# Optimization experiments

Hardware: AMD Instinct MI355X
Metric: run time of the kernel (lower is better)

The kernel has to match this reference:

```python
import jax, jax.numpy as jnp
import numpy as np

B, C_IN, N = 16, 64, 8192
C_OUT, NUM_RING = 128, 8
EPS = 1e-5  # BatchNorm1d default


def setup_inputs() -> dict:
    key = jax.random.key(0)
    k1, k2, k3, k4 = jax.random.split(key, 4)
    x = jax.random.normal(k1, (B, C_IN, N), dtype=jnp.float32)
    ring = jax.random.randint(k2, (B, N), 0, NUM_RING, dtype=jnp.int32)
    W = jax.random.normal(k3, (NUM_RING, C_OUT, C_IN), dtype=jnp.float32) * 0.05
    b = jax.random.normal(k4, (NUM_RING, C_OUT), dtype=jnp.float32) * 0.05
    gamma = jnp.ones((NUM_RING, C_OUT), dtype=jnp.float32)
    beta = jnp.zeros((NUM_RING, C_OUT), dtype=jnp.float32)
    return {"x": x, "ring": ring, "W": W, "b": b, "gamma": gamma, "beta": beta}


def reference(x, ring, W, b, gamma, beta):
    Bb, C, Nn = x.shape
    num_ring = W.shape[0]
    M = Bb * Nn
    xf = x.transpose(0, 2, 1).reshape(M, C)      # [M, 64] point features
    rf = ring.reshape(M)                          # [M] ring id per point

    # Per-ring Conv1d(64->128, k=1): linear with ring-selected weights.
    # num_ring is small; masked dense GEMMs avoid gathering [M,128,64] weights.
    y = jnp.zeros((M, W.shape[1]), dtype=xf.dtype)
    for r in range(num_ring):
        yr = xf @ W[r].T + b[r]
        y = jnp.where((rf == r)[:, None], yr, y)  # [M, 128]

    # Training-mode BatchNorm1d per ring group: stats over all points of that
    # ring across all batches (BN sees [1,128,M_r]). Biased variance.
    cnt = jax.ops.segment_sum(jnp.ones((M,), y.dtype), rf, num_segments=num_ring)
    cnt = jnp.maximum(cnt, 1.0)[:, None]          # [R,1]
    s = jax.ops.segment_sum(y, rf, num_segments=num_ring)       # [R,128]
    ss = jax.ops.segment_sum(y * y, rf, num_segments=num_ring)  # [R,128]
    mean = s / cnt
    var = ss / cnt - mean * mean
    yn = (y - mean[rf]) * jax.lax.rsqrt(var[rf] + EPS) * gamma[rf] + beta[rf]

    # Segment max over (batch, ring) pairs, broadcast back to every point.
    bidx = jnp.repeat(jnp.arange(Bb, dtype=rf.dtype), Nn)        # [M]
    seg = bidx * num_ring + rf
    mx = jax.ops.segment_max(yn, seg, num_segments=Bb * num_ring)  # [B*R,128]
    out = mx[seg].reshape(Bb, Nn, -1).transpose(0, 2, 1)         # [B,128,N]
    return out
```

## Files before the change

kernel.cpp:

```cpp
#include <hip/hip_runtime.h>
#include <stdint.h>
#include <math.h>

#define B_    16
#define CIN   64
#define NPT   8192
#define COUT  128
#define NRING 8
#define EPSV  1e-5f
#define CAP   2048u
#define MBLK  6

typedef unsigned int uint32;
typedef unsigned short ushort;
typedef unsigned long long ull;
typedef short short8 __attribute__((ext_vector_type(8)));
typedef float floatx4 __attribute__((ext_vector_type(4)));

__device__ __forceinline__ uint32 fkey(float f) {
  uint32 u = __float_as_uint(f);
  return (u & 0x80000000u) ? ~u : (u | 0x80000000u);
}
__device__ __forceinline__ float kinv(uint32 k) {
  uint32 u = (k & 0x80000000u) ? (k ^ 0x80000000u) : ~k;
  return __uint_as_float(u);
}
__device__ __forceinline__ uint32 f2bf(float f) {
  uint32 u = __float_as_uint(f);
  return (u + 0x7fffu + ((u >> 16) & 1u)) >> 16;
}

__global__ __launch_bounds__(256) void k_init(
    const float* __restrict__ W, ushort* __restrict__ Wb,
    uint32* __restrict__ cursor,
    float* __restrict__ sums, float* __restrict__ ssums,
    uint32* __restrict__ mxkey, uint32* __restrict__ mnkey)
{
  int tid = threadIdx.x;
  int blk = blockIdx.x;
  if (blk < 32) {
    int idx0 = blk * 256 + tid;
    for (int idx = idx0; idx < B_ * NRING * COUT; idx += 32 * 256) {
      mxkey[idx] = 0u;
      mnkey[idx] = 0xFFFFFFFFu;
      if (idx < NRING * COUT) { sums[idx] = 0.f; ssums[idx] = 0.f; }
      if (idx < B_ * NRING)   cursor[idx] = (uint32)idx * CAP;
    }
  } else {
    int idx0 = (blk - 32) * 256 + tid;
    for (int idx = idx0; idx < NRING * COUT * CIN; idx += 8 * 256)
      Wb[idx] = (ushort)f2bf(W[idx]);
  }
}

__global__ __launch_bounds__(128) void k_scatter(
    const float* __restrict__ x, const int* __restrict__ ring,
    uint32* __restrict__ cursor, ushort* __restrict__ xsb)
{
  __shared__ uint32 xl2[64 * 33];
  __shared__ int    dstrow[64];
  __shared__ ushort rankl[64];
  __shared__ uint32 rcnt[NRING], rbase[NRING], rstart[NRING];

  int tid  = threadIdx.x;
  int lane = tid & 63;
  int w    = tid >> 6;
  int blk  = blockIdx.x;
  int b    = blk >> 7;
  int n0   = (blk & 127) * 64;

  if (w == 0) {
    int rl = ring[b * NPT + n0 + lane];
    uint32 wrank = 0;
    #pragma unroll
    for (int rr = 0; rr < NRING; ++rr) {
      ull m = __ballot(rl == rr);
      if (rl == rr) wrank = (uint32)__popcll(m & ((1ull << lane) - 1ull));
      if (lane == rr) rcnt[rr] = (uint32)__popcll(m);
    }
    if (lane < NRING) {
      rbase[lane] = atomicAdd(&cursor[b * NRING + lane], rcnt[lane]);
      uint32 s = 0;
      for (int rp = 0; rp < lane; ++rp) s += rcnt[rp];
      rstart[lane] = s;
    }
    int myrow = (int)(rstart[rl] + wrank);
    rankl[lane] = (ushort)myrow;
    uint32 gpos = rbase[rl] + wrank;
    uint32 limit = (uint32)(b * NRING + rl + 1) * CAP;
    dstrow[myrow] = (gpos < limit) ? (int)gpos : -1;
  }
  __syncthreads();

  const float* xb = x + (size_t)b * CIN * NPT + n0;
  uint32 myrank = rankl[lane];
  #pragma unroll
  for (int kp = 0; kp < 16; ++kp) {
    int k = w * 32 + kp * 2;
    float fa = xb[(size_t)k * NPT + lane];
    float fb = xb[(size_t)(k + 1) * NPT + lane];
    xl2[myrank * 33 + (k >> 1)] = f2bf(fa) | (f2bf(fb) << 16);
  }
  __syncthreads();

  uint2* dst = reinterpret_cast<uint2*>(xsb);
  #pragma unroll
  for (int i = 0; i < 8; ++i) {
    int w2 = tid + i * 128;
    int row = w2 >> 4;
    int p   = w2 & 15;
    int dr  = dstrow[row];
    if (dr >= 0) {
      uint2 v;
      v.x = xl2[row * 33 + 2 * p];
      v.y = xl2[row * 33 + 2 * p + 1];
      dst[(size_t)dr * 16 + p] = v;
    }
  }
}

__global__ __launch_bounds__(256) void k_main(
    const ushort* __restrict__ xsb, const ushort* __restrict__ Wb,
    const uint32* __restrict__ cursor,
    float* __restrict__ sums, float* __restrict__ ssums,
    uint32* __restrict__ mxkey, uint32* __restrict__ mnkey)
{
  int blk = blockIdx.x;
  int c4 = blk % MBLK;
  int r  = (blk / MBLK) & 7;
  int b  = blk / (MBLK * NRING);
  uint32 segBase = (uint32)(b * NRING + r) * CAP;
  uint32 segCnt  = __builtin_amdgcn_readfirstlane(
                       min(cursor[b * NRING + r] - segBase, CAP));

  int tid = threadIdx.x;
  int lane = tid & 63;
  int w = tid >> 6;
  uint32 m0 = (uint32)(c4 * 4 + w) * 64;
  if (m0 >= segCnt) return;

  int lm = lane & 15;
  int lk = lane >> 4;

  const ushort* wr = Wb + (size_t)r * COUT * CIN;
  short8 bfr[8][2];
  #pragma unroll
  for (int nt = 0; nt < 8; ++nt) {
    const ushort* wc = wr + (size_t)(nt * 16 + lm) * CIN + lk * 8;
    bfr[nt][0] = *reinterpret_cast<const short8*>(wc);
    bfr[nt][1] = *reinterpret_cast<const short8*>(wc + 32);
  }

  float s_[8], ss_[8], mx_[8], mn_[8];
  #pragma unroll
  for (int nt = 0; nt < 8; ++nt) {
    s_[nt] = 0.f; ss_[nt] = 0.f;
    mx_[nt] = -__builtin_inff(); mn_[nt] = __builtin_inff();
  }

  #pragma unroll
  for (int mt = 0; mt < 4; ++mt) {
    uint32 row_rel = m0 + (uint32)mt * 16 + (uint32)lm;
    bool valid = row_rel < segCnt;
    uint32 row_g = segBase + (valid ? row_rel : (segCnt - 1));
    const ushort* xr = xsb + (size_t)row_g * CIN + lk * 8;
    short8 a0 = *reinterpret_cast<const short8*>(xr);
    short8 a1 = *reinterpret_cast<const short8*>(xr + 32);
    if (!valid) { a0 = (short8)0; a1 = (short8)0; }

    #pragma unroll
    for (int nt = 0; nt < 8; ++nt) {
      floatx4 f = {0.f, 0.f, 0.f, 0.f};
      f = __builtin_amdgcn_mfma_f32_16x16x32_bf16(a0, bfr[nt][0], f, 0, 0, 0);
      f = __builtin_amdgcn_mfma_f32_16x16x32_bf16(a1, bfr[nt][1], f, 0, 0, 0);
      #pragma unroll
      for (int j = 0; j < 4; ++j) {
        bool vj = (m0 + (uint32)mt * 16 + (uint32)(lk * 4 + j)) < segCnt;
        float zv = f[j];
        s_[nt] += zv;
        ss_[nt] = fmaf(zv, zv, ss_[nt]);
        mx_[nt] = fmaxf(mx_[nt], vj ? zv : -__builtin_inff());
        mn_[nt] = fminf(mn_[nt], vj ? zv :  __builtin_inff());
      }
    }
  }

  #pragma unroll
  for (int nt = 0; nt < 8; ++nt) {
    float sv = s_[nt], qv = ss_[nt], Mv = mx_[nt], mv = mn_[nt];
    sv += __shfl_xor(sv, 16, 64); sv += __shfl_xor(sv, 32, 64);
    qv += __shfl_xor(qv, 16, 64); qv += __shfl_xor(qv, 32, 64);
    Mv = fmaxf(Mv, __shfl_xor(Mv, 16, 64)); Mv = fmaxf(Mv, __shfl_xor(Mv, 32, 64));
    mv = fminf(mv, __shfl_xor(mv, 16, 64)); mv = fminf(mv, __shfl_xor(mv, 32, 64));
    if (lane < 16) {
      int ch = nt * 16 + lane;
      atomicAdd(&sums [r * COUT + ch], sv);
      atomicAdd(&ssums[r * COUT + ch], qv);
      atomicMax(&mxkey[(b * NRING + r) * COUT + ch], fkey(Mv));
      atomicMin(&mnkey[(b * NRING + r) * COUT + ch], fkey(mv));
    }
  }
}

__global__ __launch_bounds__(256) void k_bcast(
    const int* __restrict__ ring, const uint32* __restrict__ cursor,
    const float* __restrict__ sums, const float* __restrict__ ssums,
    const uint32* __restrict__ mxkey, const uint32* __restrict__ mnkey,
    const float* __restrict__ gamma, const float* __restrict__ beta,
    float* __restrict__ out)
{
  __shared__ float mxl[NRING * 129];
  __shared__ float ringcnt[NRING];
  int tid = threadIdx.x;
  int blk = blockIdx.x;
  int b   = blk >> 7;
  int n0  = (blk & 127) * 64;

  if (tid < NRING) {
    uint32 t = 0;
    for (int bb = 0; bb < B_; ++bb)
      t += min(cursor[bb * NRING + tid] - (uint32)(bb * NRING + tid) * CAP, CAP);
    ringcnt[tid] = fmaxf((float)t, 1.f);
  }
  __syncthreads();

  for (int j = tid; j < NRING * COUT; j += 256) {
    int r = j >> 7, c = j & 127;
    float cnt  = ringcnt[r];
    float mean = sums[j] / cnt;
    float var  = fmaxf(ssums[j] / cnt - mean * mean, 0.f);
    float inv  = 1.f / sqrtf(var + EPSV);
    float a    = gamma[j] * inv;
    float bet  = beta[j];
    float zmax = kinv(mxkey[b * NRING * COUT + j]);
    float zmin = kinv(mnkey[b * NRING * COUT + j]);
    mxl[r * 129 + c] = (a >= 0.f) ? fmaf(a, zmax - mean, bet)
                                  : fmaf(a, zmin - mean, bet);
  }
  __syncthreads();

  int wv = tid >> 6, lane = tid & 63;
  int rl = ring[b * NPT + n0 + lane];
  float* ob = out + (size_t)b * COUT * NPT + n0 + lane;
  int roff = rl * 129;
  #pragma unroll 8
  for (int c = wv * 32; c < wv * 32 + 32; ++c) {
    ob[(size_t)c * NPT] = mxl[roff + c];
  }
}

extern "C" void kernel_launch(void* const* d_in, const int* in_sizes, int n_in,
                              void* d_out, int out_size, void* d_ws, size_t ws_size,
                              hipStream_t stream)
{
  const float* x     = (const float*)d_in[0];
  const int*   ring  = (const int*)  d_in[1];
  const float* W     = (const float*)d_in[2];
  const float* gamma = (const float*)d_in[4];
  const float* beta  = (const float*)d_in[5];
  float* out = (float*)d_out;

  ushort* Wb      = (ushort*)d_ws;
  uint32* cursor  = (uint32*)(Wb + 65536);
  float*  sums    = (float*)(cursor + 128);
  float*  ssums   = sums + 1024;
  uint32* mxkey   = (uint32*)(ssums + 1024);
  uint32* mnkey   = mxkey + 16384;

  ushort* xsb = (ushort*)out;

  k_init   <<<dim3(40),   dim3(256), 0, stream>>>(W, Wb, cursor, sums, ssums, mxkey, mnkey);
  k_scatter<<<dim3(2048), dim3(128), 0, stream>>>(x, ring, cursor, xsb);
  k_main   <<<dim3(B_ * NRING * MBLK), dim3(256), 0, stream>>>(xsb, Wb, cursor, sums, ssums, mxkey, mnkey);
  k_bcast  <<<dim3(2048), dim3(256), 0, stream>>>(ring, cursor, sums, ssums, mxkey, mnkey, gamma, beta, out);
}
```

Baseline: 63.35 us.

## Widen scatter and broadcast tiles to 256 points with vectorized float4 accesses

The scatter kernel now handles 256 points per block with 256 threads. Ring ranks are combined across four wavefronts through shared per-wave counts and offsets, so there are fewer cursor atomics per point. Global loads of x, stores of the bf16 rows, and the broadcast kernel's output writes now use 16-byte vector accesses. The broadcast kernel recomputes its BN/max table per block, and with 4x fewer blocks that redundant work shrinks. In exchange, shared-memory scatter writes may hit more bank conflicts, and the larger per-block LDS footprint lowers occupancy.

```diff
diff --git a/kernel.cpp b/kernel.cpp
--- a/kernel.cpp
+++ b/kernel.cpp
@@ -53,68 +53,89 @@
   }
 }
 
-__global__ __launch_bounds__(128) void k_scatter(
+__global__ __launch_bounds__(256) void k_scatter(
     const float* __restrict__ x, const int* __restrict__ ring,
     uint32* __restrict__ cursor, ushort* __restrict__ xsb)
 {
-  __shared__ uint32 xl2[64 * 33];
-  __shared__ int    dstrow[64];
-  __shared__ ushort rankl[64];
-  __shared__ uint32 rcnt[NRING], rbase[NRING], rstart[NRING];
+  __shared__ uint32 xl2[256 * 33];
+  __shared__ int    dstrow[256];
+  __shared__ ushort rankl[256];
+  __shared__ uint32 wcnt[4][NRING], woff[4][NRING];
+  __shared__ uint32 rbase[NRING], rstart[NRING];
 
   int tid  = threadIdx.x;
   int lane = tid & 63;
   int w    = tid >> 6;
   int blk  = blockIdx.x;
-  int b    = blk >> 7;
-  int n0   = (blk & 127) * 64;
-
-  if (w == 0) {
-    int rl = ring[b * NPT + n0 + lane];
-    uint32 wrank = 0;
-    #pragma unroll
+  int b    = blk >> 5;
+  int n0   = (blk & 31) * 256;
+
+  int rl = ring[b * NPT + n0 + tid];
+  uint32 wrank = 0, mycnt = 0;
+  #pragma unroll
+  for (int rr = 0; rr < NRING; ++rr) {
+    ull m = __ballot(rl == rr);
+    if (rl == rr) wrank = (uint32)__popcll(m & ((1ull << lane) - 1ull));
+    if (lane == rr) mycnt = (uint32)__popcll(m);
+  }
+  if (lane < NRING) wcnt[w][lane] = mycnt;
+  __syncthreads();
+  if (tid < NRING) {
+    uint32 t = wcnt[0][tid] + wcnt[1][tid] + wcnt[2][tid] + wcnt[3][tid];
+    rbase[tid] = atomicAdd(&cursor[b * NRING + tid], t);
+  }
+  if (tid == 0) {
+    uint32 acc = 0;
     for (int rr = 0; rr < NRING; ++rr) {
-      ull m = __ballot(rl == rr);
-      if (rl == rr) wrank = (uint32)__popcll(m & ((1ull << lane) - 1ull));
-      if (lane == rr) rcnt[rr] = (uint32)__popcll(m);
-    }
-    if (lane < NRING) {
-      rbase[lane] = atomicAdd(&cursor[b * NRING + lane], rcnt[lane]);
-      uint32 s = 0;
-      for (int rp = 0; rp < lane; ++rp) s += rcnt[rp];
-      rstart[lane] = s;
-    }
-    int myrow = (int)(rstart[rl] + wrank);
-    rankl[lane] = (ushort)myrow;
-    uint32 gpos = rbase[rl] + wrank;
+      rstart[rr] = acc;
+      uint32 o = acc;
+      #pragma unroll
+      for (int ww = 0; ww < 4; ++ww) { woff[ww][rr] = o; o += wcnt[ww][rr]; }
+      acc = o;
+    }
+  }
+  __syncthreads();
+  int myrow = (int)(woff[w][rl] + wrank);
+  rankl[tid] = (ushort)myrow;
+  {
+    uint32 gpos = rbase[rl] + ((uint32)myrow - rstart[rl]);
     uint32 limit = (uint32)(b * NRING + rl + 1) * CAP;
     dstrow[myrow] = (gpos < limit) ? (int)gpos : -1;
   }
   __syncthreads();
 
+  int myr0 = rankl[lane * 4 + 0];
+  int myr1 = rankl[lane * 4 + 1];
+  int myr2 = rankl[lane * 4 + 2];
+  int myr3 = rankl[lane * 4 + 3];
   const float* xb = x + (size_t)b * CIN * NPT + n0;
-  uint32 myrank = rankl[lane];
-  #pragma unroll
-  for (int kp = 0; kp < 16; ++kp) {
-    int k = w * 32 + kp * 2;
-    float fa = xb[(size_t)k * NPT + lane];
-    float fb = xb[(size_t)(k + 1) * NPT + lane];
-    xl2[myrank * 33 + (k >> 1)] = f2bf(fa) | (f2bf(fb) << 16);
-  }
-  __syncthreads();
-
-  uint2* dst = reinterpret_cast<uint2*>(xsb);
-  #pragma unroll
-  for (int i = 0; i < 8; ++i) {
-    int w2 = tid + i * 128;
-    int row = w2 >> 4;
-    int p   = w2 & 15;
+  #pragma unroll
+  for (int kp = 0; kp < 8; ++kp) {
+    int k0 = w * 16 + kp * 2;
+    float4 va = *reinterpret_cast<const float4*>(xb + (size_t)k0 * NPT + lane * 4);
+    float4 vb = *reinterpret_cast<const float4*>(xb + (size_t)(k0 + 1) * NPT + lane * 4);
+    int idx = k0 >> 1;
+    xl2[myr0 * 33 + idx] = f2bf(va.x) | (f2bf(vb.x) << 16);
+    xl2[myr1 * 33 + idx] = f2bf(va.y) | (f2bf(vb.y) << 16);
+    xl2[myr2 * 33 + idx] = f2bf(va.z) | (f2bf(vb.z) << 16);
+    xl2[myr3 * 33 + idx] = f2bf(va.w) | (f2bf(vb.w) << 16);
+  }
+  __syncthreads();
+
+  uint4* dst = reinterpret_cast<uint4*>(xsb);
+  #pragma unroll
+  for (int it = 0; it < 8; ++it) {
+    int slot = tid + it * 256;
+    int row = slot >> 3;
+    int p   = slot & 7;
     int dr  = dstrow[row];
     if (dr >= 0) {
-      uint2 v;
-      v.x = xl2[row * 33 + 2 * p];
-      v.y = xl2[row * 33 + 2 * p + 1];
-      dst[(size_t)dr * 16 + p] = v;
+      uint4 v;
+      v.x = xl2[row * 33 + 4 * p + 0];
+      v.y = xl2[row * 33 + 4 * p + 1];
+      v.z = xl2[row * 33 + 4 * p + 2];
+      v.w = xl2[row * 33 + 4 * p + 3];
+      dst[(size_t)dr * 8 + p] = v;
     }
   }
 }
@@ -213,8 +234,8 @@
   __shared__ float ringcnt[NRING];
   int tid = threadIdx.x;
   int blk = blockIdx.x;
-  int b   = blk >> 7;
-  int n0  = (blk & 127) * 64;
+  int b   = blk >> 5;
+  int n0  = (blk & 31) * 256;
 
   if (tid < NRING) {
     uint32 t = 0;
@@ -225,7 +246,7 @@
   __syncthreads();
 
   for (int j = tid; j < NRING * COUT; j += 256) {
-    int r = j >> 7, c = j & 127;
+    int r = j >> 7;
     float cnt  = ringcnt[r];
     float mean = sums[j] / cnt;
     float var  = fmaxf(ssums[j] / cnt - mean * mean, 0.f);
@@ -234,18 +255,24 @@
     float bet  = beta[j];
     float zmax = kinv(mxkey[b * NRING * COUT + j]);
     float zmin = kinv(mnkey[b * NRING * COUT + j]);
-    mxl[r * 129 + c] = (a >= 0.f) ? fmaf(a, zmax - mean, bet)
-                                  : fmaf(a, zmin - mean, bet);
+    mxl[r * 129 + (j & 127)] = (a >= 0.f) ? fmaf(a, zmax - mean, bet)
+                                          : fmaf(a, zmin - mean, bet);
   }
   __syncthreads();
 
   int wv = tid >> 6, lane = tid & 63;
-  int rl = ring[b * NPT + n0 + lane];
-  float* ob = out + (size_t)b * COUT * NPT + n0 + lane;
-  int roff = rl * 129;
+  int nb = n0 + lane * 4;
+  int4 r4 = *reinterpret_cast<const int4*>(&ring[b * NPT + nb]);
+  int ro0 = r4.x * 129, ro1 = r4.y * 129, ro2 = r4.z * 129, ro3 = r4.w * 129;
+  float* ob = out + (size_t)b * COUT * NPT + nb;
   #pragma unroll 8
   for (int c = wv * 32; c < wv * 32 + 32; ++c) {
-    ob[(size_t)c * NPT] = mxl[roff + c];
+    float4 v;
+    v.x = mxl[ro0 + c];
+    v.y = mxl[ro1 + c];
+    v.z = mxl[ro2 + c];
+    v.w = mxl[ro3 + c];
+    *reinterpret_cast<float4*>(ob + (size_t)c * NPT) = v;
   }
 }
 
@@ -269,8 +296,8 @@
 
   ushort* xsb = (ushort*)out;
 
-  k_init   <<<dim3(40),   dim3(256), 0, stream>>>(W, Wb, cursor, sums, ssums, mxkey, mnkey);
-  k_scatter<<<dim3(2048), dim3(128), 0, stream>>>(x, ring, cursor, xsb);
+  k_init   <<<dim3(40),  dim3(256), 0, stream>>>(W, Wb, cursor, sums, ssums, mxkey, mnkey);
+  k_scatter<<<dim3(512), dim3(256), 0, stream>>>(x, ring, cursor, xsb);
   k_main   <<<dim3(B_ * NRING * MBLK), dim3(256), 0, stream>>>(xsb, Wb, cursor, sums, ssums, mxkey, mnkey);
-  k_bcast  <<<dim3(2048), dim3(256), 0, stream>>>(ring, cursor, sums, ssums, mxkey, mnkey, gamma, beta, out);
-}
+  k_bcast  <<<dim3(512), dim3(256), 0, stream>>>(ring, cursor, sums, ssums, mxkey, mnkey, gamma, beta, out);
+}
```

Result: slower. 77.59 us (+22.5%).
